# Kernel optimization log

Hardware: AMD Instinct MI355X
Metric: run time of the kernel (lower is better)

Reference implementation:

```python
import jax, jax.numpy as jnp
import numpy as np

D_MODEL = 1024
N_HEADS = 16
HEAD_DIM = D_MODEL // N_HEADS


def setup_inputs() -> dict:
    key = jax.random.key(0)
    ks = jax.random.split(key, 9)
    s = 1.0 / np.sqrt(D_MODEL)
    x = jax.random.normal(ks[0], (2, 2048, D_MODEL), dtype=jnp.float32)
    Wq = jax.random.uniform(ks[1], (D_MODEL, D_MODEL), jnp.float32, -s, s)
    bq = jax.random.uniform(ks[2], (D_MODEL,), jnp.float32, -s, s)
    Wk = jax.random.uniform(ks[3], (D_MODEL, D_MODEL), jnp.float32, -s, s)
    bk = jax.random.uniform(ks[4], (D_MODEL,), jnp.float32, -s, s)
    Wv = jax.random.uniform(ks[5], (D_MODEL, D_MODEL), jnp.float32, -s, s)
    bv = jax.random.uniform(ks[6], (D_MODEL,), jnp.float32, -s, s)
    Wo = jax.random.uniform(ks[7], (D_MODEL, D_MODEL), jnp.float32, -s, s)
    bo = jax.random.uniform(ks[8], (D_MODEL,), jnp.float32, -s, s)
    return {"x": x, "Wq": Wq, "bq": bq, "Wk": Wk, "bk": bk,
            "Wv": Wv, "bv": bv, "Wo": Wo, "bo": bo}


def reference(x, Wq, bq, Wk, bk, Wv, bv, Wo, bo):
    B, S, _ = x.shape
    # project and split heads: [B, H, S, Dh]
    def heads(W, b):
        return (x @ W + b).reshape(B, S, N_HEADS, HEAD_DIM).transpose(0, 2, 1, 3)
    Q, K, V = heads(Wq, bq), heads(Wk, bk), heads(Wv, bv)
    scale = 1.0 / np.sqrt(HEAD_DIM).astype(np.float32)
    scores = jnp.einsum('bhsd,bhtd->bhst', Q, K) * scale  # [B,H,S,S]
    causal = jnp.tril(jnp.ones((S, S), dtype=bool))
    scores = jnp.where(causal, scores, -jnp.inf)
    attn = jax.nn.softmax(scores, axis=-1)
    out = jnp.einsum('bhst,bhtd->bhsd', attn, V)  # [B,H,S,Dh]
    out = out.transpose(0, 2, 1, 3).reshape(B, S, D_MODEL)
    return out @ Wo + bo
```

## Files before the change

### kernel.cpp

```cpp
#include <hip/hip_runtime.h>

typedef __attribute__((ext_vector_type(8))) __bf16 bfrag;
typedef __attribute__((ext_vector_type(4))) float f32x4;

#define MFMA(a, b, c) __builtin_amdgcn_mfma_f32_16x16x32_bf16((a), (b), (c), 0, 0, 0)

#define D_MODEL 1024
#define SEQ     2048
#define NB      2
#define NH      16
#define HD      64
#define MROWS   (NB * SEQ)

#define SCALE_LOG2 0.18033688011112043f
#define NEG_BIG    (-3.0e38f)

#define GLOBAL_AS(p) ((const __attribute__((address_space(1))) void*)(p))
#define LDS_AS(p)    ((__attribute__((address_space(3))) void*)(p))
#define ASYNC_CP16(g, l) __builtin_amdgcn_global_load_lds(GLOBAL_AS(g), LDS_AS(l), 16, 0, 0)

__global__ __launch_bounds__(256) void k_prep(
    const float* __restrict__ x,
    const float* __restrict__ Wq, const float* __restrict__ Wk,
    const float* __restrict__ Wv, const float* __restrict__ Wo,
    __bf16* __restrict__ Wt, __bf16* __restrict__ xb)
{
    __shared__ __bf16 t[64][65];
    if (blockIdx.z == 4) {
        size_t base = ((size_t)(blockIdx.y * 16 + blockIdx.x)) * 16384;
        for (int j = 0; j < 8; ++j) {
            size_t i = base + (size_t)j * 2048 + (size_t)threadIdx.x * 8;
            float4 f0 = *(const float4*)&x[i];
            float4 f1 = *(const float4*)&x[i + 4];
            union { uint4 u; __bf16 h[8]; } cv;
            cv.h[0] = (__bf16)f0.x; cv.h[1] = (__bf16)f0.y;
            cv.h[2] = (__bf16)f0.z; cv.h[3] = (__bf16)f0.w;
            cv.h[4] = (__bf16)f1.x; cv.h[5] = (__bf16)f1.y;
            cv.h[6] = (__bf16)f1.z; cv.h[7] = (__bf16)f1.w;
            *(uint4*)&xb[i] = cv.u;
        }
        return;
    }
    const float* src = (blockIdx.z == 0) ? Wq : (blockIdx.z == 1) ? Wk
                      : (blockIdx.z == 2) ? Wv : Wo;
    __bf16* dst = Wt + (size_t)blockIdx.z * (1024u * 1024u);
    int tr = blockIdx.y * 64, tc = blockIdx.x * 64;
    for (int j = 0; j < 16; ++j) {
        int id = threadIdx.x + j * 256;
        int r = id >> 6, c = id & 63;
        t[r][c] = (__bf16)src[(size_t)(tr + r) * 1024 + tc + c];
    }
    __syncthreads();
    for (int j = 0; j < 2; ++j) {
        int id = threadIdx.x + j * 256;
        int r = id >> 3;
        int c8 = (id & 7) * 8;
        union { uint4 u; __bf16 h[8]; } pk;
        for (int i = 0; i < 8; ++i) pk.h[i] = t[c8 + i][r];
        *(uint4*)&dst[(size_t)(tc + r) * 1024 + tr + c8] = pk.u;
    }
}

template <int MODE, bool WT>
__global__ __launch_bounds__(256) void k_gemm128(
    const void* __restrict__ Ap,
    const void* __restrict__ W0, const void* __restrict__ W1,
    const void* __restrict__ W2,
    const float* __restrict__ b0, const float* __restrict__ b1,
    const float* __restrict__ b2, void* __restrict__ dstp)
{
    constexpr int AST = WT ? 64 : 72;
    alignas(16) __shared__ __bf16 SH[18432];
    __bf16* As = SH;
    __bf16* Bs = SH + 128 * AST;

    const int tid = threadIdx.x;
    const int z = blockIdx.z;
    const int m0 = blockIdx.y * 128;
    const int n0 = blockIdx.x * 128;
    const void* W     = (z == 0) ? W0 : (z == 1) ? W1 : W2;
    const float* bias = (z == 0) ? b0 : (z == 1) ? b1 : b2;

    const int wid = tid >> 6, lane = tid & 63;
    const int quad = lane >> 4, l16 = lane & 15;
    const int wRow = (wid >> 1) * 64, wCol = (wid & 1) * 64;

    f32x4 acc[4][4];
    const f32x4 zero = {0.f, 0.f, 0.f, 0.f};
    for (int mi = 0; mi < 4; ++mi)
        for (int ni = 0; ni < 4; ++ni) acc[mi][ni] = zero;

    const int srow = tid >> 3;
    const int sseg = (tid & 7) * 8;
    const int bkrow = tid >> 4;
    const int bnseg = (tid & 15) * 8;
    const int arow = lane >> 3;
    const int akoff = ((lane & 7) * 8) ^ (arow * 8);
    const int sw = (l16 & 7) * 8;

    for (int k0 = 0; k0 < D_MODEL; k0 += 64) {
        __syncthreads();
        if (WT) {
            const __bf16* Ab = (const __bf16*)Ap;
            const __bf16* Bt = (const __bf16*)W;
            for (int it = 0; it < 4; ++it) {
                int row = wid * 32 + it * 8;
                ASYNC_CP16(&Ab[(size_t)(m0 + row + arow) * D_MODEL + k0 + akoff],
                           &As[row * 64]);
                ASYNC_CP16(&Bt[(size_t)(n0 + row + arow) * D_MODEL + k0 + akoff],
                           &Bs[row * 64]);
            }
        } else {
            if (MODE == 0) {
                const float* A = (const float*)Ap;
                for (int it = 0; it < 4; ++it) {
                    int row = srow + it * 32;
                    const float* src = &A[(size_t)(m0 + row) * D_MODEL + k0 + sseg];
                    float4 f0 = *(const float4*)src;
                    float4 f1 = *(const float4*)(src + 4);
                    union { uint4 u; __bf16 h[8]; } cv;
                    cv.h[0] = (__bf16)f0.x; cv.h[1] = (__bf16)f0.y;
                    cv.h[2] = (__bf16)f0.z; cv.h[3] = (__bf16)f0.w;
                    cv.h[4] = (__bf16)f1.x; cv.h[5] = (__bf16)f1.y;
                    cv.h[6] = (__bf16)f1.z; cv.h[7] = (__bf16)f1.w;
                    *(uint4*)&As[row * AST + sseg] = cv.u;
                }
            } else {
                const __bf16* A = (const __bf16*)Ap;
                for (int it = 0; it < 4; ++it) {
                    int row = srow + it * 32;
                    uint4 va = *(const uint4*)&A[(size_t)(m0 + row) * D_MODEL + k0 + sseg];
                    *(uint4*)&As[row * AST + sseg] = va;
                }
            }
            const float* Wf = (const float*)W;
            for (int it = 0; it < 4; ++it) {
                int krow = bkrow + it * 16;
                const float* src = &Wf[(size_t)(k0 + krow) * D_MODEL + n0 + bnseg];
                float4 f0 = *(const float4*)src;
                float4 f1 = *(const float4*)(src + 4);
                Bs[(bnseg + 0) * AST + krow] = (__bf16)f0.x;
                Bs[(bnseg + 1) * AST + krow] = (__bf16)f0.y;
                Bs[(bnseg + 2) * AST + krow] = (__bf16)f0.z;
                Bs[(bnseg + 3) * AST + krow] = (__bf16)f0.w;
                Bs[(bnseg + 4) * AST + krow] = (__bf16)f1.x;
                Bs[(bnseg + 5) * AST + krow] = (__bf16)f1.y;
                Bs[(bnseg + 6) * AST + krow] = (__bf16)f1.z;
                Bs[(bnseg + 7) * AST + krow] = (__bf16)f1.w;
            }
        }
        __syncthreads();
        for (int kk = 0; kk < 64; kk += 32) {
            bfrag af[4], bf[4];
            if (WT) {
                int ko = (kk + quad * 8) ^ sw;
                for (int mi = 0; mi < 4; ++mi)
                    af[mi] = *(const bfrag*)&As[(wRow + mi * 16 + l16) * 64 + ko];
                for (int ni = 0; ni < 4; ++ni)
                    bf[ni] = *(const bfrag*)&Bs[(wCol + ni * 16 + l16) * 64 + ko];
            } else {
                for (int mi = 0; mi < 4; ++mi)
                    af[mi] = *(const bfrag*)&As[(wRow + mi * 16 + l16) * AST + kk + quad * 8];
                for (int ni = 0; ni < 4; ++ni)
                    bf[ni] = *(const bfrag*)&Bs[(wCol + ni * 16 + l16) * AST + kk + quad * 8];
            }
            for (int mi = 0; mi < 4; ++mi)
                for (int ni = 0; ni < 4; ++ni)
                    acc[mi][ni] = MFMA(af[mi], bf[ni], acc[mi][ni]);
        }
    }

    if (MODE == 0) {
        float biasv[4];
        for (int ni = 0; ni < 4; ++ni) biasv[ni] = bias[n0 + wCol + ni * 16 + l16];
        const int b = m0 >> 11, m0s = m0 & 2047, h0 = n0 >> 6;
        __syncthreads();
        if (z < 2) {
            for (int mi = 0; mi < 4; ++mi)
                for (int ni = 0; ni < 4; ++ni) {
                    int col = wCol + ni * 16 + l16;
                    for (int r = 0; r < 4; ++r) {
                        float v = acc[mi][ni][r] + biasv[ni];
                        if (z == 0) v *= SCALE_LOG2;
                        SH[(wRow + mi * 16 + quad * 4 + r) * 136 + col] = (__bf16)v;
                    }
                }
            __syncthreads();
            __bf16* qk = (__bf16*)dstp + (size_t)z * (MROWS * (size_t)D_MODEL);
            for (int i = 0; i < 8; ++i) {
                int rid = i * 32 + (tid >> 3);
                int hl = rid >> 7, sl = rid & 127;
                int dcol = (tid & 7) * 8;
                uint4 v = *(const uint4*)&SH[sl * 136 + hl * 64 + dcol];
                *(uint4*)&qk[(((size_t)b * NH + h0 + hl) * SEQ + m0s + sl) * HD + dcol] = v;
            }
        } else {
            for (int mi = 0; mi < 4; ++mi)
                for (int ni = 0; ni < 4; ++ni) {
                    int col = wCol + ni * 16 + l16;
                    int s0 = wRow + mi * 16 + quad * 4;
                    union { unsigned long long u; __bf16 h4[4]; } pk;
                    for (int r = 0; r < 4; ++r)
                        pk.h4[r] = (__bf16)(acc[mi][ni][r] + biasv[ni]);
                    *(unsigned long long*)&SH[col * 136 + s0] = pk.u;
                }
            __syncthreads();
            __bf16* vv = (__bf16*)dstp + (size_t)2 * (MROWS * (size_t)D_MODEL);
            for (int i = 0; i < 8; ++i) {
                int rid = i * 16 + (tid >> 4);
                int hl = rid >> 6, d = rid & 63;
                int sc = (tid & 15) * 8;
                uint4 v = *(const uint4*)&SH[rid * 136 + sc];
                *(uint4*)&vv[(((size_t)b * NH + h0 + hl) * HD + d) * SEQ + m0s + sc] = v;
            }
        }
    } else {
        for (int mi = 0; mi < 4; ++mi)
            for (int ni = 0; ni < 4; ++ni) {
                int gn = n0 + wCol + ni * 16 + l16;
                float bv = bias[gn];
                for (int r = 0; r < 4; ++r) {
                    int gm = m0 + wRow + mi * 16 + quad * 4 + r;
                    ((float*)dstp)[(size_t)gm * D_MODEL + gn] = acc[mi][ni][r] + bv;
                }
            }
    }
}

__global__ __launch_bounds__(256) void k_gemm_out(
    const __bf16* __restrict__ A, const __bf16* __restrict__ Bt,
    const float* __restrict__ bias, float* __restrict__ dst)
{
    alignas(16) __shared__ __bf16 As[64 * 64];
    alignas(16) __shared__ __bf16 Bs[128 * 64];

    const int tid = threadIdx.x;
    const int m0 = blockIdx.y * 64;
    const int n0 = blockIdx.x * 128;
    const int wid = tid >> 6, lane = tid & 63;
    const int quad = lane >> 4, l16 = lane & 15;
    const int wRow = (wid >> 1) * 32, wCol = (wid & 1) * 64;

    f32x4 acc[2][4];
    const f32x4 zero = {0.f, 0.f, 0.f, 0.f};
    for (int mi = 0; mi < 2; ++mi)
        for (int ni = 0; ni < 4; ++ni) acc[mi][ni] = zero;

    const int arow = lane >> 3;
    const int akoff = ((lane & 7) * 8) ^ (arow * 8);
    const int sw = (l16 & 7) * 8;

    for (int k0 = 0; k0 < D_MODEL; k0 += 64) {
        __syncthreads();
        for (int it = 0; it < 2; ++it) {
            int row = wid * 16 + it * 8;
            ASYNC_CP16(&A[(size_t)(m0 + row + arow) * D_MODEL + k0 + akoff],
                       &As[row * 64]);
        }
        for (int it = 0; it < 4; ++it) {
            int row = wid * 32 + it * 8;
            ASYNC_CP16(&Bt[(size_t)(n0 + row + arow) * D_MODEL + k0 + akoff],
                       &Bs[row * 64]);
        }
        __syncthreads();
        for (int kk = 0; kk < 64; kk += 32) {
            int ko = (kk + quad * 8) ^ sw;
            bfrag af[2], bf[4];
            for (int mi = 0; mi < 2; ++mi)
                af[mi] = *(const bfrag*)&As[(wRow + mi * 16 + l16) * 64 + ko];
            for (int ni = 0; ni < 4; ++ni)
                bf[ni] = *(const bfrag*)&Bs[(wCol + ni * 16 + l16) * 64 + ko];
            for (int mi = 0; mi < 2; ++mi)
                for (int ni = 0; ni < 4; ++ni)
                    acc[mi][ni] = MFMA(af[mi], bf[ni], acc[mi][ni]);
        }
    }

    for (int mi = 0; mi < 2; ++mi)
        for (int ni = 0; ni < 4; ++ni) {
            int gn = n0 + wCol + ni * 16 + l16;
            float bv = bias[gn];
            for (int r = 0; r < 4; ++r) {
                int gm = m0 + wRow + mi * 16 + quad * 4 + r;
                dst[(size_t)gm * D_MODEL + gn] = acc[mi][ni][r] + bv;
            }
        }
}

__global__ __launch_bounds__(256) void k_attn(
    const __bf16* __restrict__ Q, const __bf16* __restrict__ K,
    const __bf16* __restrict__ Vt, __bf16* __restrict__ O)
{
    alignas(16) __shared__ __bf16 Ks[64 * 64];
    alignas(16) __shared__ __bf16 Vts[64 * 64];
    alignas(16) __shared__ __bf16 Ps[4][16 * 64];

    const int tid = threadIdx.x, wid = tid >> 6, lane = tid & 63;
    const int quad = lane >> 4, l16 = lane & 15;
    const int u = (blockIdx.x + blockIdx.y + 16 * blockIdx.z) & 31;
    const int qb = (u & 1) ? 31 - (u >> 1) : (u >> 1);
    const int h = blockIdx.y, b = blockIdx.z;
    const size_t bh = ((size_t)b * NH + h) * SEQ * HD;
    const __bf16* Qg  = Q + bh + (size_t)qb * 64 * HD;
    const __bf16* Kg  = K + bh;
    const __bf16* Vtg = Vt + ((size_t)b * NH + h) * HD * SEQ;

    bfrag qf[2];
    qf[0] = *(const bfrag*)&Qg[(size_t)(wid * 16 + l16) * HD + quad * 8];
    qf[1] = *(const bfrag*)&Qg[(size_t)(wid * 16 + l16) * HD + 32 + quad * 8];

    const f32x4 zero = {0.f, 0.f, 0.f, 0.f};
    f32x4 o[4];
    for (int dt = 0; dt < 4; ++dt) o[dt] = zero;
    float lrow = 0.f;
    const int q = qb * 64 + wid * 16 + l16;
    const int srcbase = (lane & 48) + quad * 4;
    const int sw = (l16 & 7) * 8;
    const int ntile = qb + 1;

    const int row0 = tid >> 3, seg = (tid & 7) * 8;
    const int sseg = seg ^ ((row0 & 7) * 8);

    uint4 kreg0 = *(const uint4*)&Kg[(size_t)row0 * HD + seg];
    uint4 kreg1 = *(const uint4*)&Kg[(size_t)(row0 + 32) * HD + seg];
    uint4 vreg0 = *(const uint4*)&Vtg[(size_t)row0 * SEQ + seg];
    uint4 vreg1 = *(const uint4*)&Vtg[(size_t)(row0 + 32) * SEQ + seg];

    for (int t = 0; t < ntile; ++t) {
        const int j0 = t * 64;
        __syncthreads();
        *(uint4*)&Ks[row0 * 64 + sseg] = kreg0;
        *(uint4*)&Ks[(row0 + 32) * 64 + sseg] = kreg1;
        *(uint4*)&Vts[row0 * 64 + sseg] = vreg0;
        *(uint4*)&Vts[(row0 + 32) * 64 + sseg] = vreg1;
        if (t + 1 < ntile) {
            const int j1 = j0 + 64;
            kreg0 = *(const uint4*)&Kg[(size_t)(j1 + row0) * HD + seg];
            kreg1 = *(const uint4*)&Kg[(size_t)(j1 + row0 + 32) * HD + seg];
            vreg0 = *(const uint4*)&Vtg[(size_t)row0 * SEQ + j1 + seg];
            vreg1 = *(const uint4*)&Vtg[(size_t)(row0 + 32) * SEQ + j1 + seg];
        }
        __syncthreads();

        f32x4 st[4];
        for (int kt = 0; kt < 4; ++kt) {
            bfrag ka0 = *(const bfrag*)&Ks[(kt * 16 + l16) * 64 + ((quad * 8) ^ sw)];
            bfrag ka1 = *(const bfrag*)&Ks[(kt * 16 + l16) * 64 + ((32 + quad * 8) ^ sw)];
            st[kt] = MFMA(ka1, qf[1], MFMA(ka0, qf[0], zero));
        }

        if (t == ntile - 1) {
            for (int kt = 0; kt < 4; ++kt)
                for (int r = 0; r < 4; ++r) {
                    float v = (j0 + kt * 16 + quad * 4 + r > q) ? NEG_BIG : st[kt][r];
                    float p = exp2f(v);
                    st[kt][r] = p;
                    lrow += p;
                }
        } else {
            for (int kt = 0; kt < 4; ++kt)
                for (int r = 0; r < 4; ++r) {
                    float p = exp2f(st[kt][r]);
                    st[kt][r] = p;
                    lrow += p;
                }
        }

        for (int kt = 0; kt < 4; ++kt) {
            union { unsigned long long u; __bf16 h4[4]; } pk;
            for (int r = 0; r < 4; ++r) pk.h4[r] = (__bf16)st[kt][r];
            *(unsigned long long*)&Ps[wid][l16 * 64 + ((kt * 16 + quad * 4) ^ sw)] = pk.u;
        }
        asm volatile("s_waitcnt lgkmcnt(0)" ::: "memory");

        for (int c = 0; c < 2; ++c) {
            int ko = (c * 32 + quad * 8) ^ sw;
            bfrag pf = *(const bfrag*)&Ps[wid][l16 * 64 + ko];
            for (int dt = 0; dt < 4; ++dt) {
                bfrag vf = *(const bfrag*)&Vts[(dt * 16 + l16) * 64 + ko];
                o[dt] = MFMA(pf, vf, o[dt]);
            }
        }
    }

    float lsum = lrow + __shfl_xor(lrow, 16, 64);
    lsum = lsum + __shfl_xor(lsum, 32, 64);
    for (int r = 0; r < 4; ++r) {
        float lr = __shfl(lsum, srcbase + r, 64);
        float inv = 1.0f / lr;
        size_t base = ((size_t)b * SEQ + qb * 64 + wid * 16 + quad * 4 + r) * D_MODEL
                    + (size_t)h * HD;
        for (int dt = 0; dt < 4; ++dt)
            O[base + dt * 16 + l16] = (__bf16)(o[dt][r] * inv);
    }
}

extern "C" void kernel_launch(void* const* d_in, const int* in_sizes, int n_in,
                              void* d_out, int out_size, void* d_ws, size_t ws_size,
                              hipStream_t stream)
{
    const float* x  = (const float*)d_in[0];
    const float* Wq = (const float*)d_in[1];
    const float* bq = (const float*)d_in[2];
    const float* Wk = (const float*)d_in[3];
    const float* bk = (const float*)d_in[4];
    const float* Wv = (const float*)d_in[5];
    const float* bv = (const float*)d_in[6];
    const float* Wo = (const float*)d_in[7];
    const float* bo = (const float*)d_in[8];

    __bf16* ws = (__bf16*)d_ws;
    const size_t M1 = 1024u * 1024u;
    __bf16* qkv    = ws;
    __bf16* attn_o = ws + 12 * M1;
    __bf16* Wt     = ws + 16 * M1;
    __bf16* xb     = ws + 20 * M1;

    const bool fast = ws_size >= (size_t)48 * 1024 * 1024;

    if (fast) {
        k_prep<<<dim3(16, 16, 5), 256, 0, stream>>>(x, Wq, Wk, Wv, Wo, Wt, xb);
        k_gemm128<0, true><<<dim3(8, 32, 3), 256, 0, stream>>>(
            xb, Wt, Wt + M1, Wt + 2 * M1, bq, bk, bv, qkv);
        k_attn<<<dim3(32, 16, 2), 256, 0, stream>>>(
            qkv, qkv + 4 * M1, qkv + 8 * M1, attn_o);
        k_gemm_out<<<dim3(8, 64), 256, 0, stream>>>(
            attn_o, Wt + 3 * M1, bo, (float*)d_out);
    } else {
        k_gemm128<0, false><<<dim3(8, 32, 3), 256, 0, stream>>>(
            x, Wq, Wk, Wv, bq, bk, bv, qkv);
        k_attn<<<dim3(32, 16, 2), 256, 0, stream>>>(
            qkv, qkv + 4 * M1, qkv + 8 * M1, attn_o);
        k_gemm128<1, false><<<dim3(8, 32, 1), 256, 0, stream>>>(
            attn_o, Wo, Wo, Wo, bo, bo, bo, (float*)d_out);
    }
}
```

Before: 198.2 us.

## Split attention KV tiles across waves with direct global loads and LDS reduction

Restructures the causal attention kernel so each block handles 32 query rows and the four waves split the key/value tiles among themselves (split-K inside the block). Each wave loads its K and V fragments straight from global memory into registers, which removes the shared K/V staging and the per-tile block barriers. Partial outputs and row sums are then combined through LDS at the end. The grid doubles to 64 query tiles, ordered longest first, with a launch-bounds occupancy hint. The risk is less K/V reuse across waves, uncoalesced fragment loads, higher register pressure, and a serial reduction tail.

New measurement: 253.8 us. 1.28x slower.

```diff
diff --git a/kernel.cpp b/kernel.cpp
--- a/kernel.cpp
+++ b/kernel.cpp
@@ -287,111 +287,150 @@
         }
 }
 
-__global__ __launch_bounds__(256) void k_attn(
+__global__ __launch_bounds__(256, 3) void k_attn(
     const __bf16* __restrict__ Q, const __bf16* __restrict__ K,
     const __bf16* __restrict__ Vt, __bf16* __restrict__ O)
 {
-    alignas(16) __shared__ __bf16 Ks[64 * 64];
-    alignas(16) __shared__ __bf16 Vts[64 * 64];
-    alignas(16) __shared__ __bf16 Ps[4][16 * 64];
+    alignas(16) __shared__ __bf16 Ps[4][2][16 * 64];
+    __shared__ float Ls[2][16][4];
 
     const int tid = threadIdx.x, wid = tid >> 6, lane = tid & 63;
     const int quad = lane >> 4, l16 = lane & 15;
-    const int u = (blockIdx.x + blockIdx.y + 16 * blockIdx.z) & 31;
-    const int qb = (u & 1) ? 31 - (u >> 1) : (u >> 1);
+    const int qt = 63 - (int)blockIdx.x;
     const int h = blockIdx.y, b = blockIdx.z;
-    const size_t bh = ((size_t)b * NH + h) * SEQ * HD;
-    const __bf16* Qg  = Q + bh + (size_t)qb * 64 * HD;
-    const __bf16* Kg  = K + bh;
+    const size_t bhq = ((size_t)b * NH + h) * SEQ * HD;
+    const int q0 = qt * 32;
+    const __bf16* Qg  = Q + bhq + (size_t)q0 * HD;
+    const __bf16* Kg  = K + bhq;
     const __bf16* Vtg = Vt + ((size_t)b * NH + h) * HD * SEQ;
-
-    bfrag qf[2];
-    qf[0] = *(const bfrag*)&Qg[(size_t)(wid * 16 + l16) * HD + quad * 8];
-    qf[1] = *(const bfrag*)&Qg[(size_t)(wid * 16 + l16) * HD + 32 + quad * 8];
+    const int ntile = (qt >> 1) + 1;
+
+    bfrag qf[2][2];
+    for (int ms = 0; ms < 2; ++ms)
+        for (int kc = 0; kc < 2; ++kc)
+            qf[ms][kc] = *(const bfrag*)&Qg[(size_t)(ms * 16 + l16) * HD
+                                            + kc * 32 + quad * 8];
 
     const f32x4 zero = {0.f, 0.f, 0.f, 0.f};
-    f32x4 o[4];
-    for (int dt = 0; dt < 4; ++dt) o[dt] = zero;
-    float lrow = 0.f;
-    const int q = qb * 64 + wid * 16 + l16;
-    const int srcbase = (lane & 48) + quad * 4;
+    f32x4 o[2][4];
+    for (int ms = 0; ms < 2; ++ms)
+        for (int dt = 0; dt < 4; ++dt) o[ms][dt] = zero;
+    float lrow[2] = {0.f, 0.f};
     const int sw = (l16 & 7) * 8;
-    const int ntile = qb + 1;
-
-    const int row0 = tid >> 3, seg = (tid & 7) * 8;
-    const int sseg = seg ^ ((row0 & 7) * 8);
-
-    uint4 kreg0 = *(const uint4*)&Kg[(size_t)row0 * HD + seg];
-    uint4 kreg1 = *(const uint4*)&Kg[(size_t)(row0 + 32) * HD + seg];
-    uint4 vreg0 = *(const uint4*)&Vtg[(size_t)row0 * SEQ + seg];
-    uint4 vreg1 = *(const uint4*)&Vtg[(size_t)(row0 + 32) * SEQ + seg];
-
-    for (int t = 0; t < ntile; ++t) {
+    __bf16* Pw = &Ps[wid][0][0];
+
+    for (int t = wid; t < ntile; t += 4) {
         const int j0 = t * 64;
-        __syncthreads();
-        *(uint4*)&Ks[row0 * 64 + sseg] = kreg0;
-        *(uint4*)&Ks[(row0 + 32) * 64 + sseg] = kreg1;
-        *(uint4*)&Vts[row0 * 64 + sseg] = vreg0;
-        *(uint4*)&Vts[(row0 + 32) * 64 + sseg] = vreg1;
-        if (t + 1 < ntile) {
-            const int j1 = j0 + 64;
-            kreg0 = *(const uint4*)&Kg[(size_t)(j1 + row0) * HD + seg];
-            kreg1 = *(const uint4*)&Kg[(size_t)(j1 + row0 + 32) * HD + seg];
-            vreg0 = *(const uint4*)&Vtg[(size_t)row0 * SEQ + j1 + seg];
-            vreg1 = *(const uint4*)&Vtg[(size_t)(row0 + 32) * SEQ + j1 + seg];
-        }
-        __syncthreads();
-
-        f32x4 st[4];
+
+        bfrag ka[4][2];
         for (int kt = 0; kt < 4; ++kt) {
-            bfrag ka0 = *(const bfrag*)&Ks[(kt * 16 + l16) * 64 + ((quad * 8) ^ sw)];
-            bfrag ka1 = *(const bfrag*)&Ks[(kt * 16 + l16) * 64 + ((32 + quad * 8) ^ sw)];
-            st[kt] = MFMA(ka1, qf[1], MFMA(ka0, qf[0], zero));
-        }
+            const __bf16* kr = &Kg[(size_t)(j0 + kt * 16 + l16) * HD + quad * 8];
+            ka[kt][0] = *(const bfrag*)kr;
+            ka[kt][1] = *(const bfrag*)(kr + 32);
+        }
+        bfrag vf[2][4];
+        for (int c = 0; c < 2; ++c)
+            for (int dt = 0; dt < 4; ++dt)
+                vf[c][dt] = *(const bfrag*)&Vtg[(size_t)(dt * 16 + l16) * SEQ
+                                                + j0 + c * 32 + quad * 8];
+
+        f32x4 st[2][4];
+        for (int ms = 0; ms < 2; ++ms)
+            for (int kt = 0; kt < 4; ++kt)
+                st[ms][kt] = MFMA(ka[kt][1], qf[ms][1],
+                                  MFMA(ka[kt][0], qf[ms][0], zero));
 
         if (t == ntile - 1) {
-            for (int kt = 0; kt < 4; ++kt)
-                for (int r = 0; r < 4; ++r) {
-                    float v = (j0 + kt * 16 + quad * 4 + r > q) ? NEG_BIG : st[kt][r];
-                    float p = exp2f(v);
-                    st[kt][r] = p;
-                    lrow += p;
-                }
+            for (int ms = 0; ms < 2; ++ms) {
+                const int qrow = q0 + ms * 16 + l16;
+                for (int kt = 0; kt < 4; ++kt)
+                    for (int r = 0; r < 4; ++r) {
+                        float v = (j0 + kt * 16 + quad * 4 + r > qrow)
+                                    ? NEG_BIG : st[ms][kt][r];
+                        float p = exp2f(v);
+                        st[ms][kt][r] = p;
+                        lrow[ms] += p;
+                    }
+            }
         } else {
-            for (int kt = 0; kt < 4; ++kt)
-                for (int r = 0; r < 4; ++r) {
-                    float p = exp2f(st[kt][r]);
-                    st[kt][r] = p;
-                    lrow += p;
-                }
-        }
-
-        for (int kt = 0; kt < 4; ++kt) {
-            union { unsigned long long u; __bf16 h4[4]; } pk;
-            for (int r = 0; r < 4; ++r) pk.h4[r] = (__bf16)st[kt][r];
-            *(unsigned long long*)&Ps[wid][l16 * 64 + ((kt * 16 + quad * 4) ^ sw)] = pk.u;
-        }
+            for (int ms = 0; ms < 2; ++ms)
+                for (int kt = 0; kt < 4; ++kt)
+                    for (int r = 0; r < 4; ++r) {
+                        float p = exp2f(st[ms][kt][r]);
+                        st[ms][kt][r] = p;
+                        lrow[ms] += p;
+                    }
+        }
+
+        for (int ms = 0; ms < 2; ++ms)
+            for (int kt = 0; kt < 4; ++kt) {
+                union { unsigned long long u; __bf16 h4[4]; } pk;
+                for (int r = 0; r < 4; ++r) pk.h4[r] = (__bf16)st[ms][kt][r];
+                *(unsigned long long*)
+                    &Pw[ms * 1024 + l16 * 64 + ((kt * 16 + quad * 4) ^ sw)] = pk.u;
+            }
         asm volatile("s_waitcnt lgkmcnt(0)" ::: "memory");
 
-        for (int c = 0; c < 2; ++c) {
-            int ko = (c * 32 + quad * 8) ^ sw;
-            bfrag pf = *(const bfrag*)&Ps[wid][l16 * 64 + ko];
-            for (int dt = 0; dt < 4; ++dt) {
-                bfrag vf = *(const bfrag*)&Vts[(dt * 16 + l16) * 64 + ko];
-                o[dt] = MFMA(pf, vf, o[dt]);
-            }
-        }
-    }
-
-    float lsum = lrow + __shfl_xor(lrow, 16, 64);
-    lsum = lsum + __shfl_xor(lsum, 32, 64);
-    for (int r = 0; r < 4; ++r) {
-        float lr = __shfl(lsum, srcbase + r, 64);
-        float inv = 1.0f / lr;
-        size_t base = ((size_t)b * SEQ + qb * 64 + wid * 16 + quad * 4 + r) * D_MODEL
-                    + (size_t)h * HD;
-        for (int dt = 0; dt < 4; ++dt)
-            O[base + dt * 16 + l16] = (__bf16)(o[dt][r] * inv);
+        for (int ms = 0; ms < 2; ++ms)
+            for (int c = 0; c < 2; ++c) {
+                int ko = (c * 32 + quad * 8) ^ sw;
+                bfrag pf = *(const bfrag*)&Pw[ms * 1024 + l16 * 64 + ko];
+                for (int dt = 0; dt < 4; ++dt)
+                    o[ms][dt] = MFMA(pf, vf[c][dt], o[ms][dt]);
+            }
+    }
+
+    for (int ms = 0; ms < 2; ++ms) {
+        float s = lrow[ms];
+        s += __shfl_xor(s, 16, 64);
+        s += __shfl_xor(s, 32, 64);
+        lrow[ms] = s;
+    }
+    if (lane < 16) {
+        Ls[0][l16][wid] = lrow[0];
+        Ls[1][l16][wid] = lrow[1];
+    }
+
+    float* R = (float*)&Ps[0][0][0];
+    __syncthreads();
+    if (wid >= 2) {
+        float* Rw = R + (wid - 2) * 2048;
+        for (int ms = 0; ms < 2; ++ms)
+            for (int dt = 0; dt < 4; ++dt)
+                for (int r = 0; r < 4; ++r)
+                    Rw[(ms * 16 + quad * 4 + r) * 64 + dt * 16 + l16] = o[ms][dt][r];
+    }
+    __syncthreads();
+    if (wid < 2) {
+        const float* Rw = R + wid * 2048;
+        for (int ms = 0; ms < 2; ++ms)
+            for (int dt = 0; dt < 4; ++dt)
+                for (int r = 0; r < 4; ++r)
+                    o[ms][dt][r] += Rw[(ms * 16 + quad * 4 + r) * 64 + dt * 16 + l16];
+    }
+    __syncthreads();
+    if (wid == 1) {
+        for (int ms = 0; ms < 2; ++ms)
+            for (int dt = 0; dt < 4; ++dt)
+                for (int r = 0; r < 4; ++r)
+                    R[(ms * 16 + quad * 4 + r) * 64 + dt * 16 + l16] = o[ms][dt][r];
+    }
+    __syncthreads();
+    if (wid == 0) {
+        for (int ms = 0; ms < 2; ++ms)
+            for (int dt = 0; dt < 4; ++dt)
+                for (int r = 0; r < 4; ++r)
+                    o[ms][dt][r] += R[(ms * 16 + quad * 4 + r) * 64 + dt * 16 + l16];
+        for (int ms = 0; ms < 2; ++ms)
+            for (int r = 0; r < 4; ++r) {
+                const int row = quad * 4 + r;
+                float4 lv = *(const float4*)&Ls[ms][row][0];
+                float inv = 1.0f / (lv.x + lv.y + lv.z + lv.w);
+                size_t base = ((size_t)b * SEQ + q0 + ms * 16 + row) * D_MODEL
+                            + (size_t)h * HD;
+                for (int dt = 0; dt < 4; ++dt)
+                    O[base + dt * 16 + l16] = (__bf16)(o[ms][dt][r] * inv);
+            }
     }
 }
 
@@ -422,14 +461,14 @@
         k_prep<<<dim3(16, 16, 5), 256, 0, stream>>>(x, Wq, Wk, Wv, Wo, Wt, xb);
         k_gemm128<0, true><<<dim3(8, 32, 3), 256, 0, stream>>>(
             xb, Wt, Wt + M1, Wt + 2 * M1, bq, bk, bv, qkv);
-        k_attn<<<dim3(32, 16, 2), 256, 0, stream>>>(
+        k_attn<<<dim3(64, 16, 2), 256, 0, stream>>>(
             qkv, qkv + 4 * M1, qkv + 8 * M1, attn_o);
         k_gemm_out<<<dim3(8, 64), 256, 0, stream>>>(
             attn_o, Wt + 3 * M1, bo, (float*)d_out);
     } else {
         k_gemm128<0, false><<<dim3(8, 32, 3), 256, 0, stream>>>(
             x, Wq, Wk, Wv, bq, bk, bv, qkv);
-        k_attn<<<dim3(32, 16, 2), 256, 0, stream>>>(
+        k_attn<<<dim3(64, 16, 2), 256, 0, stream>>>(
             qkv, qkv + 4 * M1, qkv + 8 * M1, attn_o);
         k_gemm128<1, false><<<dim3(8, 32, 1), 256, 0, stream>>>(
             attn_o, Wo, Wo, Wo, bo, bo, bo, (float*)d_out);
```

## Split long causal attention query blocks across two workgroups with combine kernel

Applied to the files above, without the earlier changes.

The causal attention kernel now splits the KV range of the 16 longest query blocks per head into two halves, each handled by a separate workgroup that writes unnormalized fp32 partial outputs and row sums to workspace. A new combine kernel adds the halves and normalizes into the bf16 output. The aim is to balance the triangular workload and shorten the tail of the longest workgroups. The cost is an extra launch plus fp32 partial traffic, and the path only runs when the workspace is at least 68 MiB. Skipping max-subtraction is safe here because exponents are unshifted in both halves.

Measured after the change: 200.8 us. Within noise of the previous version (+1.3%).

```diff
diff --git a/kernel.cpp b/kernel.cpp
--- a/kernel.cpp
+++ b/kernel.cpp
@@ -287,9 +287,11 @@
         }
 }
 
+template <bool SPLIT>
 __global__ __launch_bounds__(256) void k_attn(
     const __bf16* __restrict__ Q, const __bf16* __restrict__ K,
-    const __bf16* __restrict__ Vt, __bf16* __restrict__ O)
+    const __bf16* __restrict__ Vt, __bf16* __restrict__ O,
+    float* __restrict__ Po, float* __restrict__ Pl)
 {
     alignas(16) __shared__ __bf16 Ks[64 * 64];
     alignas(16) __shared__ __bf16 Vts[64 * 64];
@@ -297,9 +299,24 @@
 
     const int tid = threadIdx.x, wid = tid >> 6, lane = tid & 63;
     const int quad = lane >> 4, l16 = lane & 15;
-    const int u = (blockIdx.x + blockIdx.y + 16 * blockIdx.z) & 31;
-    const int qb = (u & 1) ? 31 - (u >> 1) : (u >> 1);
     const int h = blockIdx.y, b = blockIdx.z;
+
+    int qb, t0, t1, hf = 0;
+    bool partial = false;
+    if (SPLIT) {
+        const int xi = blockIdx.x;
+        if (xi < 32) {
+            qb = 31 - (xi >> 1); hf = xi & 1;
+            const int n = qb + 1, nh = (n + 1) >> 1;
+            t0 = hf ? nh : 0; t1 = hf ? n : nh;
+            partial = true;
+        } else { qb = 47 - xi; t0 = 0; t1 = qb + 1; }
+    } else {
+        const int u = (blockIdx.x + blockIdx.y + 16 * blockIdx.z) & 31;
+        qb = (u & 1) ? 31 - (u >> 1) : (u >> 1);
+        t0 = 0; t1 = qb + 1;
+    }
+
     const size_t bh = ((size_t)b * NH + h) * SEQ * HD;
     const __bf16* Qg  = Q + bh + (size_t)qb * 64 * HD;
     const __bf16* Kg  = K + bh;
@@ -316,24 +333,23 @@
     const int q = qb * 64 + wid * 16 + l16;
     const int srcbase = (lane & 48) + quad * 4;
     const int sw = (l16 & 7) * 8;
-    const int ntile = qb + 1;
 
     const int row0 = tid >> 3, seg = (tid & 7) * 8;
     const int sseg = seg ^ ((row0 & 7) * 8);
 
-    uint4 kreg0 = *(const uint4*)&Kg[(size_t)row0 * HD + seg];
-    uint4 kreg1 = *(const uint4*)&Kg[(size_t)(row0 + 32) * HD + seg];
-    uint4 vreg0 = *(const uint4*)&Vtg[(size_t)row0 * SEQ + seg];
-    uint4 vreg1 = *(const uint4*)&Vtg[(size_t)(row0 + 32) * SEQ + seg];
-
-    for (int t = 0; t < ntile; ++t) {
+    uint4 kreg0 = *(const uint4*)&Kg[(size_t)(t0 * 64 + row0) * HD + seg];
+    uint4 kreg1 = *(const uint4*)&Kg[(size_t)(t0 * 64 + row0 + 32) * HD + seg];
+    uint4 vreg0 = *(const uint4*)&Vtg[(size_t)row0 * SEQ + t0 * 64 + seg];
+    uint4 vreg1 = *(const uint4*)&Vtg[(size_t)(row0 + 32) * SEQ + t0 * 64 + seg];
+
+    for (int t = t0; t < t1; ++t) {
         const int j0 = t * 64;
         __syncthreads();
         *(uint4*)&Ks[row0 * 64 + sseg] = kreg0;
         *(uint4*)&Ks[(row0 + 32) * 64 + sseg] = kreg1;
         *(uint4*)&Vts[row0 * 64 + sseg] = vreg0;
         *(uint4*)&Vts[(row0 + 32) * 64 + sseg] = vreg1;
-        if (t + 1 < ntile) {
+        if (t + 1 < t1) {
             const int j1 = j0 + 64;
             kreg0 = *(const uint4*)&Kg[(size_t)(j1 + row0) * HD + seg];
             kreg1 = *(const uint4*)&Kg[(size_t)(j1 + row0 + 32) * HD + seg];
@@ -349,7 +365,7 @@
             st[kt] = MFMA(ka1, qf[1], MFMA(ka0, qf[0], zero));
         }
 
-        if (t == ntile - 1) {
+        if (t == qb) {
             for (int kt = 0; kt < 4; ++kt)
                 for (int r = 0; r < 4; ++r) {
                     float v = (j0 + kt * 16 + quad * 4 + r > q) ? NEG_BIG : st[kt][r];
@@ -385,14 +401,45 @@
 
     float lsum = lrow + __shfl_xor(lrow, 16, 64);
     lsum = lsum + __shfl_xor(lsum, 32, 64);
-    for (int r = 0; r < 4; ++r) {
-        float lr = __shfl(lsum, srcbase + r, 64);
-        float inv = 1.0f / lr;
-        size_t base = ((size_t)b * SEQ + qb * 64 + wid * 16 + quad * 4 + r) * D_MODEL
-                    + (size_t)h * HD;
-        for (int dt = 0; dt < 4; ++dt)
-            O[base + dt * 16 + l16] = (__bf16)(o[dt][r] * inv);
-    }
+
+    if (!partial) {
+        for (int r = 0; r < 4; ++r) {
+            float lr = __shfl(lsum, srcbase + r, 64);
+            float inv = 1.0f / lr;
+            size_t base = ((size_t)b * SEQ + qb * 64 + wid * 16 + quad * 4 + r) * D_MODEL
+                        + (size_t)h * HD;
+            for (int dt = 0; dt < 4; ++dt)
+                O[base + dt * 16 + l16] = (__bf16)(o[dt][r] * inv);
+        }
+    } else {
+        const int p = (((b * NH + h) * 16) + (qb - 16)) * 2 + hf;
+        float* po = Po + (size_t)p * 4096;
+        for (int r = 0; r < 4; ++r) {
+            int row = wid * 16 + quad * 4 + r;
+            for (int dt = 0; dt < 4; ++dt)
+                po[row * 64 + dt * 16 + l16] = o[dt][r];
+        }
+        if (quad == 0) Pl[(size_t)p * 64 + wid * 16 + l16] = lsum;
+    }
+}
+
+__global__ __launch_bounds__(256) void k_attn_comb(
+    const float* __restrict__ Po, const float* __restrict__ Pl,
+    __bf16* __restrict__ O)
+{
+    const int qb = 16 + blockIdx.x, h = blockIdx.y, b = blockIdx.z;
+    const int p0 = (((b * NH + h) * 16) + blockIdx.x) * 2;
+    const float* o0 = Po + (size_t)p0 * 4096;
+    const float* o1 = o0 + 4096;
+    const int tid = threadIdx.x;
+    const int row = tid >> 2, c0 = (tid & 3) * 16;
+    const float inv = 1.0f / (Pl[(size_t)p0 * 64 + row] + Pl[(size_t)p0 * 64 + 64 + row]);
+    union { uint4 u[2]; __bf16 hh[16]; } pk;
+    for (int i = 0; i < 16; ++i)
+        pk.hh[i] = (__bf16)((o0[row * 64 + c0 + i] + o1[row * 64 + c0 + i]) * inv);
+    size_t base = ((size_t)b * SEQ + qb * 64 + row) * D_MODEL + (size_t)h * HD + c0;
+    *(uint4*)&O[base] = pk.u[0];
+    *(uint4*)&O[base + 8] = pk.u[1];
 }
 
 extern "C" void kernel_launch(void* const* d_in, const int* in_sizes, int n_in,
@@ -415,22 +462,31 @@
     __bf16* attn_o = ws + 12 * M1;
     __bf16* Wt     = ws + 16 * M1;
     __bf16* xb     = ws + 20 * M1;
-
-    const bool fast = ws_size >= (size_t)48 * 1024 * 1024;
+    float*  Po     = (float*)(ws + 24 * M1);
+    float*  Pl     = (float*)(ws + 32 * M1);
+
+    const bool fast  = ws_size >= (size_t)48 * 1024 * 1024;
+    const bool split = ws_size >= (size_t)68 * 1024 * 1024;
 
     if (fast) {
         k_prep<<<dim3(16, 16, 5), 256, 0, stream>>>(x, Wq, Wk, Wv, Wo, Wt, xb);
         k_gemm128<0, true><<<dim3(8, 32, 3), 256, 0, stream>>>(
             xb, Wt, Wt + M1, Wt + 2 * M1, bq, bk, bv, qkv);
-        k_attn<<<dim3(32, 16, 2), 256, 0, stream>>>(
-            qkv, qkv + 4 * M1, qkv + 8 * M1, attn_o);
+        if (split) {
+            k_attn<true><<<dim3(48, 16, 2), 256, 0, stream>>>(
+                qkv, qkv + 4 * M1, qkv + 8 * M1, attn_o, Po, Pl);
+            k_attn_comb<<<dim3(16, 16, 2), 256, 0, stream>>>(Po, Pl, attn_o);
+        } else {
+            k_attn<false><<<dim3(32, 16, 2), 256, 0, stream>>>(
+                qkv, qkv + 4 * M1, qkv + 8 * M1, attn_o, nullptr, nullptr);
+        }
         k_gemm_out<<<dim3(8, 64), 256, 0, stream>>>(
             attn_o, Wt + 3 * M1, bo, (float*)d_out);
     } else {
         k_gemm128<0, false><<<dim3(8, 32, 3), 256, 0, stream>>>(
             x, Wq, Wk, Wv, bq, bk, bv, qkv);
-        k_attn<<<dim3(32, 16, 2), 256, 0, stream>>>(
-            qkv, qkv + 4 * M1, qkv + 8 * M1, attn_o);
+        k_attn<false><<<dim3(32, 16, 2), 256, 0, stream>>>(
+            qkv, qkv + 4 * M1, qkv + 8 * M1, attn_o, nullptr, nullptr);
         k_gemm128<1, false><<<dim3(8, 32, 1), 256, 0, stream>>>(
             attn_o, Wo, Wo, Wo, bo, bo, bo, (float*)d_out);
     }
```

## Use 128-row causal attention tiles with split-KV halves and a combine kernel

Applied to the files above, without the earlier changes.

Adds a new attention kernel in which each block handles 128 query rows (32 per wave), which doubles reuse of each K/V tile loaded into LDS. For the eight longest query blocks, the causal KV range is split into two halves run by separate blocks. These blocks write unnormalised fp32 partial outputs and row sums to workspace, and a small combine kernel merges them, which balances the triangular workload. The new path needs a larger workspace (at least 68 MB), so it falls back to the old 64-row kernel otherwise. It also adds one extra launch and a round trip of fp32 partials through global memory.

Measured after the change: 255.8 us. 1.29x slower.

```diff
diff --git a/kernel.cpp b/kernel.cpp
--- a/kernel.cpp
+++ b/kernel.cpp
@@ -287,7 +287,181 @@
         }
 }
 
-__global__ __launch_bounds__(256) void k_attn(
+__global__ __launch_bounds__(256, 4) void k_attn128(
+    const __bf16* __restrict__ Q, const __bf16* __restrict__ K,
+    const __bf16* __restrict__ Vt, __bf16* __restrict__ O,
+    float* __restrict__ Po, float* __restrict__ Pl)
+{
+    alignas(16) __shared__ __bf16 Ks[64 * 64];
+    alignas(16) __shared__ __bf16 Vts[64 * 64];
+    alignas(16) __shared__ __bf16 Ps[4][2][16 * 64];
+
+    const int tid = threadIdx.x, wid = tid >> 6, lane = tid & 63;
+    const int quad = lane >> 4, l16 = lane & 15;
+    const int h = blockIdx.y, b = blockIdx.z;
+
+    int qb, t0, t1, hf = 0;
+    bool partial = false;
+    {
+        const int xi = blockIdx.x;
+        if (xi < 16) {
+            qb = 15 - (xi >> 1); hf = xi & 1;
+            const int n = 2 * qb + 2, nh = n >> 1;
+            t0 = hf ? nh : 0; t1 = hf ? n : nh;
+            partial = true;
+        } else { qb = 23 - xi; t0 = 0; t1 = 2 * qb + 2; }
+    }
+
+    const size_t bh = ((size_t)b * NH + h) * SEQ * HD;
+    const __bf16* Qg  = Q + bh + (size_t)qb * 128 * HD;
+    const __bf16* Kg  = K + bh;
+    const __bf16* Vtg = Vt + ((size_t)b * NH + h) * HD * SEQ;
+
+    const int qlo = qb * 128 + wid * 32;
+
+    bfrag qf[2][2];
+    for (int ms = 0; ms < 2; ++ms)
+        for (int kc = 0; kc < 2; ++kc)
+            qf[ms][kc] = *(const bfrag*)&Qg[(size_t)(wid * 32 + ms * 16 + l16) * HD
+                                            + kc * 32 + quad * 8];
+
+    const f32x4 zero = {0.f, 0.f, 0.f, 0.f};
+    f32x4 o[2][4];
+    for (int ms = 0; ms < 2; ++ms)
+        for (int dt = 0; dt < 4; ++dt) o[ms][dt] = zero;
+    float lrow[2] = {0.f, 0.f};
+    const int srcbase = (lane & 48) + quad * 4;
+    const int sw = (l16 & 7) * 8;
+    __bf16* Pw = &Ps[wid][0][0];
+
+    const int row0 = tid >> 3, seg = (tid & 7) * 8;
+    const int sseg = seg ^ ((row0 & 7) * 8);
+
+    uint4 kreg0 = *(const uint4*)&Kg[(size_t)(t0 * 64 + row0) * HD + seg];
+    uint4 kreg1 = *(const uint4*)&Kg[(size_t)(t0 * 64 + row0 + 32) * HD + seg];
+    uint4 vreg0 = *(const uint4*)&Vtg[(size_t)row0 * SEQ + t0 * 64 + seg];
+    uint4 vreg1 = *(const uint4*)&Vtg[(size_t)(row0 + 32) * SEQ + t0 * 64 + seg];
+
+    for (int t = t0; t < t1; ++t) {
+        const int j0 = t * 64;
+        __syncthreads();
+        *(uint4*)&Ks[row0 * 64 + sseg] = kreg0;
+        *(uint4*)&Ks[(row0 + 32) * 64 + sseg] = kreg1;
+        *(uint4*)&Vts[row0 * 64 + sseg] = vreg0;
+        *(uint4*)&Vts[(row0 + 32) * 64 + sseg] = vreg1;
+        if (t + 1 < t1) {
+            const int j1 = j0 + 64;
+            kreg0 = *(const uint4*)&Kg[(size_t)(j1 + row0) * HD + seg];
+            kreg1 = *(const uint4*)&Kg[(size_t)(j1 + row0 + 32) * HD + seg];
+            vreg0 = *(const uint4*)&Vtg[(size_t)row0 * SEQ + j1 + seg];
+            vreg1 = *(const uint4*)&Vtg[(size_t)(row0 + 32) * SEQ + j1 + seg];
+        }
+        __syncthreads();
+
+        if (j0 > qlo + 31) continue;
+
+        f32x4 st[2][4];
+        for (int kt = 0; kt < 4; ++kt) {
+            bfrag ka0 = *(const bfrag*)&Ks[(kt * 16 + l16) * 64 + ((quad * 8) ^ sw)];
+            bfrag ka1 = *(const bfrag*)&Ks[(kt * 16 + l16) * 64 + ((32 + quad * 8) ^ sw)];
+            st[0][kt] = MFMA(ka1, qf[0][1], MFMA(ka0, qf[0][0], zero));
+            st[1][kt] = MFMA(ka1, qf[1][1], MFMA(ka0, qf[1][0], zero));
+        }
+
+        if (j0 + 63 > qlo) {
+            for (int ms = 0; ms < 2; ++ms) {
+                const int q = qlo + ms * 16 + l16;
+                for (int kt = 0; kt < 4; ++kt)
+                    for (int r = 0; r < 4; ++r) {
+                        float v = (j0 + kt * 16 + quad * 4 + r > q)
+                                    ? NEG_BIG : st[ms][kt][r];
+                        float p = exp2f(v);
+                        st[ms][kt][r] = p;
+                        lrow[ms] += p;
+                    }
+            }
+        } else {
+            for (int ms = 0; ms < 2; ++ms)
+                for (int kt = 0; kt < 4; ++kt)
+                    for (int r = 0; r < 4; ++r) {
+                        float p = exp2f(st[ms][kt][r]);
+                        st[ms][kt][r] = p;
+                        lrow[ms] += p;
+                    }
+        }
+
+        for (int ms = 0; ms < 2; ++ms)
+            for (int kt = 0; kt < 4; ++kt) {
+                union { unsigned long long u; __bf16 h4[4]; } pk;
+                for (int r = 0; r < 4; ++r) pk.h4[r] = (__bf16)st[ms][kt][r];
+                *(unsigned long long*)
+                    &Pw[ms * 1024 + l16 * 64 + ((kt * 16 + quad * 4) ^ sw)] = pk.u;
+            }
+        asm volatile("s_waitcnt lgkmcnt(0)" ::: "memory");
+
+        for (int c = 0; c < 2; ++c) {
+            const int ko = (c * 32 + quad * 8) ^ sw;
+            bfrag pf0 = *(const bfrag*)&Pw[0 * 1024 + l16 * 64 + ko];
+            bfrag pf1 = *(const bfrag*)&Pw[1 * 1024 + l16 * 64 + ko];
+            for (int dt = 0; dt < 4; ++dt) {
+                bfrag vf = *(const bfrag*)&Vts[(dt * 16 + l16) * 64 + ko];
+                o[0][dt] = MFMA(pf0, vf, o[0][dt]);
+                o[1][dt] = MFMA(pf1, vf, o[1][dt]);
+            }
+        }
+    }
+
+    float lsum[2];
+    for (int ms = 0; ms < 2; ++ms) {
+        float s = lrow[ms] + __shfl_xor(lrow[ms], 16, 64);
+        lsum[ms] = s + __shfl_xor(s, 32, 64);
+    }
+
+    if (!partial) {
+        for (int ms = 0; ms < 2; ++ms)
+            for (int r = 0; r < 4; ++r) {
+                float lr = __shfl(lsum[ms], srcbase + r, 64);
+                float inv = 1.0f / lr;
+                size_t base = ((size_t)b * SEQ + qlo + ms * 16 + quad * 4 + r) * D_MODEL
+                            + (size_t)h * HD;
+                for (int dt = 0; dt < 4; ++dt)
+                    O[base + dt * 16 + l16] = (__bf16)(o[ms][dt][r] * inv);
+            }
+    } else {
+        const int p = (((b * NH + h) * 8) + (qb - 8)) * 2 + hf;
+        float* po = Po + (size_t)p * 8192;
+        for (int ms = 0; ms < 2; ++ms)
+            for (int r = 0; r < 4; ++r) {
+                int row = wid * 32 + ms * 16 + quad * 4 + r;
+                for (int dt = 0; dt < 4; ++dt)
+                    po[row * 64 + dt * 16 + l16] = o[ms][dt][r];
+            }
+        if (quad == 0)
+            for (int ms = 0; ms < 2; ++ms)
+                Pl[(size_t)p * 128 + wid * 32 + ms * 16 + l16] = lsum[ms];
+    }
+}
+
+__global__ __launch_bounds__(256) void k_attn_comb(
+    const float* __restrict__ Po, const float* __restrict__ Pl,
+    __bf16* __restrict__ O)
+{
+    const int qb = 8 + blockIdx.x, h = blockIdx.y, b = blockIdx.z;
+    const int p0 = (((b * NH + h) * 8) + blockIdx.x) * 2;
+    const float* o0 = Po + (size_t)p0 * 8192;
+    const float* o1 = o0 + 8192;
+    const int tid = threadIdx.x;
+    const int row = tid >> 1, c0 = (tid & 1) * 32;
+    const float inv = 1.0f / (Pl[(size_t)p0 * 128 + row] + Pl[(size_t)p0 * 128 + 128 + row]);
+    union { uint4 u[4]; __bf16 hh[32]; } pk;
+    for (int i = 0; i < 32; ++i)
+        pk.hh[i] = (__bf16)((o0[row * 64 + c0 + i] + o1[row * 64 + c0 + i]) * inv);
+    size_t base = ((size_t)b * SEQ + qb * 128 + row) * D_MODEL + (size_t)h * HD + c0;
+    for (int j = 0; j < 4; ++j)
+        *(uint4*)&O[base + j * 8] = pk.u[j];
+}
+
+__global__ __launch_bounds__(256) void k_attn64(
     const __bf16* __restrict__ Q, const __bf16* __restrict__ K,
     const __bf16* __restrict__ Vt, __bf16* __restrict__ O)
 {
@@ -415,21 +589,30 @@
     __bf16* attn_o = ws + 12 * M1;
     __bf16* Wt     = ws + 16 * M1;
     __bf16* xb     = ws + 20 * M1;
-
-    const bool fast = ws_size >= (size_t)48 * 1024 * 1024;
+    float*  Po     = (float*)(ws + 24 * M1);
+    float*  Pl     = (float*)(ws + 32 * M1);
+
+    const bool fast  = ws_size >= (size_t)48 * 1024 * 1024;
+    const bool split = ws_size >= (size_t)68 * 1024 * 1024;
 
     if (fast) {
         k_prep<<<dim3(16, 16, 5), 256, 0, stream>>>(x, Wq, Wk, Wv, Wo, Wt, xb);
         k_gemm128<0, true><<<dim3(8, 32, 3), 256, 0, stream>>>(
             xb, Wt, Wt + M1, Wt + 2 * M1, bq, bk, bv, qkv);
-        k_attn<<<dim3(32, 16, 2), 256, 0, stream>>>(
-            qkv, qkv + 4 * M1, qkv + 8 * M1, attn_o);
+        if (split) {
+            k_attn128<<<dim3(24, 16, 2), 256, 0, stream>>>(
+                qkv, qkv + 4 * M1, qkv + 8 * M1, attn_o, Po, Pl);
+            k_attn_comb<<<dim3(8, 16, 2), 256, 0, stream>>>(Po, Pl, attn_o);
+        } else {
+            k_attn64<<<dim3(32, 16, 2), 256, 0, stream>>>(
+                qkv, qkv + 4 * M1, qkv + 8 * M1, attn_o);
+        }
         k_gemm_out<<<dim3(8, 64), 256, 0, stream>>>(
             attn_o, Wt + 3 * M1, bo, (float*)d_out);
     } else {
         k_gemm128<0, false><<<dim3(8, 32, 3), 256, 0, stream>>>(
             x, Wq, Wk, Wv, bq, bk, bv, qkv);
-        k_attn<<<dim3(32, 16, 2), 256, 0, stream>>>(
+        k_attn64<<<dim3(32, 16, 2), 256, 0, stream>>>(
             qkv, qkv + 4 * M1, qkv + 8 * M1, attn_o);
         k_gemm128<1, false><<<dim3(8, 32, 1), 256, 0, stream>>>(
             attn_o, Wo, Wo, Wo, bo, bo, bo, (float*)d_out);
```
